# Performance work log

Measured on AMD Instinct MI355X. Metric: run time of the kernel, lower is better.

Reference implementation:

```python
import jax, jax.numpy as jnp
import numpy as np

D_IN = 2048
D_OUT = 2048
NUM_HEADS = 16
NUM_GROUPS = 4
HEAD_DIM = D_OUT // NUM_HEADS          # 128
HEADS_PER_GROUP = NUM_HEADS // NUM_GROUPS  # 4


def setup_inputs() -> dict:
    key = jax.random.key(0)
    ks = jax.random.split(key, 6)
    b, s = 2, 2048
    x = jax.random.normal(ks[0], (b, s, D_IN), dtype=jnp.float32)
    # Store weights as [in, out] so y = x @ W (equivalent to torch Linear x @ W.T)
    sc_q = 1.0 / np.sqrt(D_IN)
    Wq = jax.random.uniform(ks[1], (D_IN, D_OUT), jnp.float32, -sc_q, sc_q)
    Wk = jax.random.uniform(ks[2], (D_IN, NUM_GROUPS * HEAD_DIM), jnp.float32, -sc_q, sc_q)
    Wv = jax.random.uniform(ks[3], (D_IN, NUM_GROUPS * HEAD_DIM), jnp.float32, -sc_q, sc_q)
    sc_o = 1.0 / np.sqrt(D_OUT)
    Wo = jax.random.uniform(ks[4], (D_OUT, D_OUT), jnp.float32, -sc_o, sc_o)
    bo = jax.random.uniform(ks[5], (D_OUT,), jnp.float32, -sc_o, sc_o)
    return {"x": x, "Wq": Wq, "Wk": Wk, "Wv": Wv, "Wo": Wo, "bo": bo}


def reference(x, Wq, Wk, Wv, Wo, bo):
    b, s, _ = x.shape
    g, hpg, hd = NUM_GROUPS, HEADS_PER_GROUP, HEAD_DIM
    # Projections; keep grouped layout instead of repeat_interleave (same math)
    q = (x @ Wq).reshape(b, s, g, hpg, hd)   # query heads ordered group-major,
                                             # matching repeat_interleave of K/V
    k = (x @ Wk).reshape(b, s, g, hd)
    v = (x @ Wv).reshape(b, s, g, hd)
    # scores: [b, g, hpg, q_len, k_len]
    scores = jnp.einsum('bqghd,bkgd->bghqk', q, k)
    causal = jnp.triu(jnp.ones((s, s), dtype=bool), k=1)  # True above diagonal
    scores = jnp.where(causal, -jnp.inf, scores)
    scale = 1.0 / jnp.sqrt(jnp.asarray(hd, dtype=scores.dtype))
    attn = jax.nn.softmax(scores * scale, axis=-1)
    ctx = jnp.einsum('bghqk,bkgd->bqghd', attn, v).reshape(b, s, D_OUT)
    return ctx @ Wo + bo
```

## Files before the change

kernel.cpp:

```cpp
#include <hip/hip_runtime.h>

typedef short v8s __attribute__((ext_vector_type(8)));
typedef float v4f __attribute__((ext_vector_type(4)));

__device__ __forceinline__ short f2bf(float f) {
  union { float f; unsigned u; } v; v.f = f;
  unsigned r = v.u + 0x7FFFu + ((v.u >> 16) & 1u);
  return (short)(r >> 16);
}

__device__ __forceinline__ void gll16(const short* g, short* l) {
  __builtin_amdgcn_global_load_lds(
      (const __attribute__((address_space(1))) void*)g,
      (__attribute__((address_space(3))) void*)l, 16, 0, 0);
}

__global__ void cast_and_transpose(const float* __restrict__ x, short* __restrict__ xb,
                                   const float* __restrict__ Wq, const float* __restrict__ Wk,
                                   const float* __restrict__ Wv, const float* __restrict__ Wo,
                                   short* __restrict__ Wqkvt, short* __restrict__ Wot) {
  const int tid = threadIdx.x;
  int bid = blockIdx.x;
  if (bid < 8192) {
    int i = bid * 256 + tid;
    float4 v = ((const float4*)x)[i];
    short4 o;
    o.x = f2bf(v.x); o.y = f2bf(v.y); o.z = f2bf(v.z); o.w = f2bf(v.w);
    ((short4*)xb)[i] = o;
    return;
  }
  __shared__ float tile[32][33];
  bid -= 8192;
  const int tx = tid & 31, ty = tid >> 5;
  int bx = bid % 160;
  const int byy = bid / 160;
  const float* src; short* dst; int C, cb;
  if (bx < 64)      { src = Wq; dst = Wqkvt;                        C = 2048; cb = bx; }
  else if (bx < 80) { src = Wk; dst = Wqkvt + (size_t)2048 * 2048;  C = 512;  cb = bx - 64; }
  else if (bx < 96) { src = Wv; dst = Wqkvt + (size_t)2560 * 2048;  C = 512;  cb = bx - 80; }
  else              { src = Wo; dst = Wot;                          C = 2048; cb = bx - 96; }
  const int c0 = cb * 32, r0 = byy * 32;
#pragma unroll
  for (int i = 0; i < 4; ++i)
    tile[ty + 8 * i][tx] = src[(size_t)(r0 + ty + 8 * i) * C + c0 + tx];
  __syncthreads();
#pragma unroll
  for (int i = 0; i < 4; ++i)
    dst[(size_t)(c0 + ty + 8 * i) * 2048 + r0 + tx] = f2bf(tile[tx][ty + 8 * i]);
}

__global__ void transpose_v_perm(const short* __restrict__ qkv, short* __restrict__ out) {
  __shared__ short tile[32][33];
  const int tx = threadIdx.x, ty = threadIdx.y;
  const int c0 = blockIdx.x * 32, r0 = blockIdx.y * 32;
  const int z = blockIdx.z;
#pragma unroll
  for (int i = 0; i < 4; ++i)
    tile[ty + 8 * i][tx] = qkv[(size_t)(z * 2048 + r0 + ty + 8 * i) * 3072 + 2560 + c0 + tx];
  __syncthreads();
#pragma unroll
  for (int i = 0; i < 4; ++i) {
    int k = r0 + tx;
    int pk = (k & ~31) | ((((k >> 2) & 3) * 2 + ((k >> 4) & 1)) * 4) | (k & 3);
    out[(size_t)z * 512 * 2048 + (size_t)(c0 + ty + 8 * i) * 2048 + pk] = tile[tx][ty + 8 * i];
  }
}

template <int BF16_OUT>
__global__ __launch_bounds__(256, 3) void gemm_bt2p(const short* __restrict__ A,
                                                    const short* __restrict__ Bt,
                                                    void* __restrict__ Cout,
                                                    const float* __restrict__ bias,
                                                    int N, int K, int nbx, int cpx) {
  __shared__ __align__(16) short sm[2 * 8192];
  const int tid = threadIdx.x;
  const int w = tid >> 6, lane = tid & 63, quad = lane >> 4, l16 = lane & 15;
  const int wm = (w >> 1) * 64, wn = (w & 1) * 64;
  const int bid = blockIdx.x;
  const int swz = (bid & 7) * cpx + (bid >> 3);
  const int n0 = (swz % nbx) * 128, m0 = (swz / nbx) * 128;
  const int NT = K >> 5;

  const int srow = lane >> 2;
  const int sc = ((lane & 3) ^ ((lane >> 2) & 3) ^ ((lane >> 4) & 3)) * 8;
  const short* Ag = A + (size_t)(m0 + w * 16 + srow) * K + sc;
  const short* Bg = Bt + (size_t)(n0 + w * 16 + srow) * K + sc;
  short* Ad = sm + w * 512 + lane * 8;
  short* Bd = sm + 4096 + w * 512 + lane * 8;
  const size_t rjump = (size_t)64 * K;

  auto stage = [&](int t, int bf_) {
    const int k = t << 5;
    short* ad = Ad + bf_ * 8192;
    short* bd = Bd + bf_ * 8192;
    gll16(Ag + k, ad);
    gll16(Ag + k + rjump, ad + 2048);
    gll16(Bg + k, bd);
    gll16(Bg + k + rjump, bd + 2048);
  };

  const int rsc = (quad ^ (l16 & 3) ^ ((l16 >> 2) & 3)) * 8;
  const short* aBase = sm + (wm + l16) * 32 + rsc;
  const short* bBase = sm + 4096 + (wn + l16) * 32 + rsc;

  v4f acc[4][4] = {};

  stage(0, 0);
  __syncthreads();

  for (int t = 0; t < NT; ++t) {
    if (t + 1 < NT) stage(t + 1, (t + 1) & 1);
    const int bo_ = (t & 1) * 8192;
    v8s af[4], bf[4];
#pragma unroll
    for (int i = 0; i < 4; ++i) af[i] = *(const v8s*)(aBase + bo_ + i * 512);
#pragma unroll
    for (int i = 0; i < 4; ++i) bf[i] = *(const v8s*)(bBase + bo_ + i * 512);
    __builtin_amdgcn_s_setprio(1);
#pragma unroll
    for (int mi = 0; mi < 4; ++mi)
#pragma unroll
      for (int ni = 0; ni < 4; ++ni)
        acc[mi][ni] = __builtin_amdgcn_mfma_f32_16x16x32_bf16(af[mi], bf[ni], acc[mi][ni], 0, 0, 0);
    __builtin_amdgcn_s_setprio(0);
    if (t + 1 < NT) __syncthreads();
  }

#pragma unroll
  for (int mi = 0; mi < 4; ++mi) {
#pragma unroll
    for (int ni = 0; ni < 4; ++ni) {
      const int col = n0 + wn + ni * 16 + l16;
#pragma unroll
      for (int r = 0; r < 4; ++r) {
        const int row = m0 + wm + mi * 16 + quad * 4 + r;
        if (BF16_OUT) {
          ((short*)Cout)[(size_t)row * N + col] = f2bf(acc[mi][ni][r]);
        } else {
          ((float*)Cout)[(size_t)row * N + col] = acc[mi][ni][r] + bias[col];
        }
      }
    }
  }
}

__global__ __launch_bounds__(256, 2) void flash_attn4(const short* __restrict__ QKV,
                                                      const short* __restrict__ Vtb,
                                                      short* __restrict__ ctx) {
  __shared__ __align__(16) short smem[32768];
  const int tid = threadIdx.x;
  const int w = tid >> 6, lane = tid & 63, quad = lane >> 4, l16 = lane & 15;
  const int wq = w >> 1, wk = w & 1;
  const int bh = blockIdx.y;
  const int b = bh >> 4, h = bh & 15, g = h >> 2;
  const float scale = 0.08838834764831845f;
  v8s ones;
#pragma unroll
  for (int i = 0; i < 8; ++i) ones[i] = (short)0x3F80;

  const int krl = lane >> 4, kcl = lane & 15;
  const int vrl = lane >> 3, vcl = lane & 7;
  const short* Kg0 = QKV + (size_t)(b * 2048 + w * 16 + krl) * 3072 + 2048 + g * 128;
  const short* Vg0 = Vtb + (size_t)(b * 512 + g * 128 + w * 32 + vrl) * 2048 + (vcl ^ (vrl & 7)) * 8;
  short* kd = smem + (w * 16) * 128 + lane * 8;
  short* vd = smem + 8192 + (w * 32) * 64 + lane * 8;

  auto stage = [&](int key0, int bs) {
    const short* kg = Kg0 + (size_t)key0 * 3072;
    const short* vg = Vg0 + key0;
#pragma unroll
    for (int ii = 0; ii < 4; ++ii) {
      const int rl = (ii * 4 + krl) & 15;
      gll16(kg + (size_t)(ii * 4) * 3072 + (kcl ^ rl) * 8, kd + bs * 16384 + ii * 512);
      gll16(vg + (size_t)(ii * 8) * 2048, vd + bs * 16384 + ii * 512);
    }
  };

  float* red = (float*)smem;

#pragma unroll 1
  for (int half = 0; half < 2; ++half) {
    const int qt = half ? (31 - blockIdx.x) : blockIdx.x;
    const int q0 = qt * 64;
    const int qb = q0 + wq * 32;

    v8s aq[2][4];
#pragma unroll
    for (int qs = 0; qs < 2; ++qs) {
      const short* Qp = QKV + (size_t)(b * 2048 + qb + qs * 16 + l16) * 3072 + h * 128 + quad * 8;
#pragma unroll
      for (int kk = 0; kk < 4; ++kk) aq[qs][kk] = *(const v8s*)(Qp + kk * 32);
    }
    v4f o[2][8] = {};
    v4f ol[2] = {};

    __syncthreads();
    stage(0, 0);
    const int nk = qt + 1;
#pragma unroll 1
    for (int kt = 0; kt < nk; ++kt) {
      const int key0 = kt << 6;
      __syncthreads();
      if (kt + 1 < nk) stage((kt + 1) << 6, (kt + 1) & 1);
      const short* Ks = smem + (kt & 1) * 16384;
      const short* Vs = Ks + 8192;
      const int kb = key0 + wk * 32;
      if (kb > qb + 31) continue;
      v4f sf[2][2] = {};
      __builtin_amdgcn_s_setprio(1);
#pragma unroll
      for (int kfl = 0; kfl < 2; ++kfl)
#pragma unroll
        for (int kk = 0; kk < 4; ++kk) {
          v8s kfr = *(const v8s*)&Ks[((wk * 2 + kfl) * 16 + l16) * 128 + (((kk * 4 + quad) ^ l16) * 8)];
#pragma unroll
          for (int qs = 0; qs < 2; ++qs)
            sf[qs][kfl] = __builtin_amdgcn_mfma_f32_16x16x32_bf16(kfr, aq[qs][kk], sf[qs][kfl], 0, 0, 0);
        }
      __builtin_amdgcn_s_setprio(0);
      const bool diag = (kb + 31 > qb);
      v8s pa[2];
#pragma unroll
      for (int qs = 0; qs < 2; ++qs) {
        const int qg = qb + qs * 16 + l16;
        v8s t;
#pragma unroll
        for (int kfl = 0; kfl < 2; ++kfl)
#pragma unroll
          for (int r = 0; r < 4; ++r) {
            float s = sf[qs][kfl][r] * scale;
            if (diag && (kb + kfl * 16 + quad * 4 + r > qg)) s = -1e30f;
            t[kfl * 4 + r] = f2bf(__expf(s));
          }
        pa[qs] = t;
      }
      __builtin_amdgcn_s_setprio(1);
#pragma unroll
      for (int nf = 0; nf < 8; ++nf) {
        v8s vf = *(const v8s*)&Vs[(nf * 16 + l16) * 64 + (((wk * 4 + quad) ^ (l16 & 7)) * 8)];
#pragma unroll
        for (int qs = 0; qs < 2; ++qs)
          o[qs][nf] = __builtin_amdgcn_mfma_f32_16x16x32_bf16(pa[qs], vf, o[qs][nf], 0, 0, 0);
      }
#pragma unroll
      for (int qs = 0; qs < 2; ++qs)
        ol[qs] = __builtin_amdgcn_mfma_f32_16x16x32_bf16(pa[qs], ones, ol[qs], 0, 0, 0);
      __builtin_amdgcn_s_setprio(0);
    }
    __syncthreads();

    if (wk == 1) {
#pragma unroll
      for (int qs = 0; qs < 2; ++qs)
        *(v4f*)&red[(wq * 2 + qs) * 256 + l16 * 16 + quad * 4] = ol[qs];
    }
    __syncthreads();
    if (wk == 0) {
#pragma unroll
      for (int qs = 0; qs < 2; ++qs)
        ol[qs] += *(const v4f*)&red[(wq * 2 + qs) * 256 + l16 * 16 + quad * 4];
    }
    __syncthreads();
    if (wk == 1) {
#pragma unroll
      for (int qs = 0; qs < 2; ++qs)
#pragma unroll
        for (int nf = 0; nf < 8; ++nf)
          *(v4f*)&red[(((wq * 2 + qs) * 8 + nf) * 256) + l16 * 16 + quad * 4] = o[qs][nf];
    }
    __syncthreads();
    if (wk == 0) {
#pragma unroll
      for (int qs = 0; qs < 2; ++qs) {
        float inv[4];
#pragma unroll
        for (int r = 0; r < 4; ++r) inv[r] = 1.0f / ol[qs][r];
#pragma unroll
        for (int nf = 0; nf < 8; ++nf) {
          v4f osum = o[qs][nf] + *(const v4f*)&red[(((wq * 2 + qs) * 8 + nf) * 256) + l16 * 16 + quad * 4];
#pragma unroll
          for (int r = 0; r < 4; ++r) {
            const int row = qb + qs * 16 + quad * 4 + r;
            ctx[(size_t)(b * 2048 + row) * 2048 + h * 128 + nf * 16 + l16] = f2bf(osum[r] * inv[r]);
          }
        }
      }
    }
  }
}

extern "C" void kernel_launch(void* const* d_in, const int* in_sizes, int n_in,
                              void* d_out, int out_size, void* d_ws, size_t ws_size,
                              hipStream_t stream) {
  const float* x = (const float*)d_in[0];
  const float* Wq = (const float*)d_in[1];
  const float* Wk = (const float*)d_in[2];
  const float* Wv = (const float*)d_in[3];
  const float* Wo = (const float*)d_in[4];
  const float* bo = (const float*)d_in[5];
  float* out = (float*)d_out;
  char* ws = (char*)d_ws;

  short* xb    = (short*)(ws);
  short* ctx   = (short*)(ws);
  short* Wqkvt = (short*)(ws + 16777216);
  short* Wot   = (short*)(ws + 29360128);
  short* QKV   = (short*)(ws + 37748736);
  short* Vtb   = (short*)(ws + 62914560);

  cast_and_transpose<<<18432, 256, 0, stream>>>(x, xb, Wq, Wk, Wv, Wo, Wqkvt, Wot);

  gemm_bt2p<1><<<768, 256, 0, stream>>>(xb, Wqkvt, (void*)QKV, nullptr, 3072, 2048, 24, 96);

  transpose_v_perm<<<dim3(16, 64, 2), dim3(32, 8), 0, stream>>>(QKV, Vtb);

  flash_attn4<<<dim3(16, 32), 256, 0, stream>>>(QKV, Vtb, ctx);

  gemm_bt2p<0><<<512, 256, 0, stream>>>(ctx, Wot, (void*)out, bo, 2048, 2048, 16, 64);
}
```

Before: 288.9 us.

## Split attention work across eight waves with 16 query rows each

The flash-attention kernel grows from 4 to 8 waves per block. Each wave now owns 16 query rows instead of 32, which halves the accumulator and Q-fragment register footprint, and the K/V staging is redistributed so each wave loads fewer rows. The aim is more resident waves per CU to hide latency. The cost is that each K/V fragment read from LDS now feeds one MFMA instead of two, roughly doubling LDS read traffic per unit of math, and there are more waves contending at each barrier. The softmax scale is also folded with log2(e) so the kernel uses exp2f.

```diff
diff --git a/kernel.cpp b/kernel.cpp
--- a/kernel.cpp
+++ b/kernel.cpp
@@ -144,7 +144,7 @@
   }
 }
 
-__global__ __launch_bounds__(256, 2) void flash_attn4(const short* __restrict__ QKV,
+__global__ __launch_bounds__(512, 4) void flash_attn6(const short* __restrict__ QKV,
                                                       const short* __restrict__ Vtb,
                                                       short* __restrict__ ctx) {
   __shared__ __align__(16) short smem[32768];
@@ -153,24 +153,24 @@
   const int wq = w >> 1, wk = w & 1;
   const int bh = blockIdx.y;
   const int b = bh >> 4, h = bh & 15, g = h >> 2;
-  const float scale = 0.08838834764831845f;
+  const float k2e = 0.08838834764831845f * 1.4426950408889634f;
   v8s ones;
 #pragma unroll
   for (int i = 0; i < 8; ++i) ones[i] = (short)0x3F80;
 
   const int krl = lane >> 4, kcl = lane & 15;
   const int vrl = lane >> 3, vcl = lane & 7;
-  const short* Kg0 = QKV + (size_t)(b * 2048 + w * 16 + krl) * 3072 + 2048 + g * 128;
-  const short* Vg0 = Vtb + (size_t)(b * 512 + g * 128 + w * 32 + vrl) * 2048 + (vcl ^ (vrl & 7)) * 8;
-  short* kd = smem + (w * 16) * 128 + lane * 8;
-  short* vd = smem + 8192 + (w * 32) * 64 + lane * 8;
+  const short* Kg0 = QKV + (size_t)(b * 2048 + w * 8 + krl) * 3072 + 2048 + g * 128;
+  const short* Vg0 = Vtb + (size_t)(b * 512 + g * 128 + w * 16 + vrl) * 2048 + (vcl ^ (vrl & 7)) * 8;
+  short* kd = smem + (w * 8) * 128 + lane * 8;
+  short* vd = smem + 8192 + (w * 16) * 64 + lane * 8;
 
   auto stage = [&](int key0, int bs) {
     const short* kg = Kg0 + (size_t)key0 * 3072;
     const short* vg = Vg0 + key0;
 #pragma unroll
-    for (int ii = 0; ii < 4; ++ii) {
-      const int rl = (ii * 4 + krl) & 15;
+    for (int ii = 0; ii < 2; ++ii) {
+      const int rl = (w & 1) * 8 + ii * 4 + krl;
       gll16(kg + (size_t)(ii * 4) * 3072 + (kcl ^ rl) * 8, kd + bs * 16384 + ii * 512);
       gll16(vg + (size_t)(ii * 8) * 2048, vd + bs * 16384 + ii * 512);
     }
@@ -182,17 +182,16 @@
   for (int half = 0; half < 2; ++half) {
     const int qt = half ? (31 - blockIdx.x) : blockIdx.x;
     const int q0 = qt * 64;
-    const int qb = q0 + wq * 32;
-
-    v8s aq[2][4];
-#pragma unroll
-    for (int qs = 0; qs < 2; ++qs) {
-      const short* Qp = QKV + (size_t)(b * 2048 + qb + qs * 16 + l16) * 3072 + h * 128 + quad * 8;
-#pragma unroll
-      for (int kk = 0; kk < 4; ++kk) aq[qs][kk] = *(const v8s*)(Qp + kk * 32);
-    }
-    v4f o[2][8] = {};
-    v4f ol[2] = {};
+    const int qb = q0 + wq * 16;
+
+    v8s aq[4];
+    {
+      const short* Qp = QKV + (size_t)(b * 2048 + qb + l16) * 3072 + h * 128 + quad * 8;
+#pragma unroll
+      for (int kk = 0; kk < 4; ++kk) aq[kk] = *(const v8s*)(Qp + kk * 32);
+    }
+    v4f o[8] = {};
+    v4f ol = {};
 
     __syncthreads();
     stage(0, 0);
@@ -205,84 +204,62 @@
       const short* Ks = smem + (kt & 1) * 16384;
       const short* Vs = Ks + 8192;
       const int kb = key0 + wk * 32;
-      if (kb > qb + 31) continue;
-      v4f sf[2][2] = {};
+      if (kb > qb + 15) continue;
+      v4f sf[2] = {};
       __builtin_amdgcn_s_setprio(1);
 #pragma unroll
       for (int kfl = 0; kfl < 2; ++kfl)
 #pragma unroll
         for (int kk = 0; kk < 4; ++kk) {
           v8s kfr = *(const v8s*)&Ks[((wk * 2 + kfl) * 16 + l16) * 128 + (((kk * 4 + quad) ^ l16) * 8)];
-#pragma unroll
-          for (int qs = 0; qs < 2; ++qs)
-            sf[qs][kfl] = __builtin_amdgcn_mfma_f32_16x16x32_bf16(kfr, aq[qs][kk], sf[qs][kfl], 0, 0, 0);
+          sf[kfl] = __builtin_amdgcn_mfma_f32_16x16x32_bf16(kfr, aq[kk], sf[kfl], 0, 0, 0);
         }
       __builtin_amdgcn_s_setprio(0);
       const bool diag = (kb + 31 > qb);
-      v8s pa[2];
-#pragma unroll
-      for (int qs = 0; qs < 2; ++qs) {
-        const int qg = qb + qs * 16 + l16;
-        v8s t;
-#pragma unroll
-        for (int kfl = 0; kfl < 2; ++kfl)
-#pragma unroll
-          for (int r = 0; r < 4; ++r) {
-            float s = sf[qs][kfl][r] * scale;
-            if (diag && (kb + kfl * 16 + quad * 4 + r > qg)) s = -1e30f;
-            t[kfl * 4 + r] = f2bf(__expf(s));
-          }
-        pa[qs] = t;
-      }
+      const int qg = qb + l16;
+      v8s pa;
+#pragma unroll
+      for (int kfl = 0; kfl < 2; ++kfl)
+#pragma unroll
+        for (int r = 0; r < 4; ++r) {
+          float s = sf[kfl][r];
+          if (diag && (kb + kfl * 16 + quad * 4 + r > qg)) s = -1e30f;
+          pa[kfl * 4 + r] = f2bf(exp2f(s * k2e));
+        }
       __builtin_amdgcn_s_setprio(1);
 #pragma unroll
       for (int nf = 0; nf < 8; ++nf) {
         v8s vf = *(const v8s*)&Vs[(nf * 16 + l16) * 64 + (((wk * 4 + quad) ^ (l16 & 7)) * 8)];
-#pragma unroll
-        for (int qs = 0; qs < 2; ++qs)
-          o[qs][nf] = __builtin_amdgcn_mfma_f32_16x16x32_bf16(pa[qs], vf, o[qs][nf], 0, 0, 0);
+        o[nf] = __builtin_amdgcn_mfma_f32_16x16x32_bf16(pa, vf, o[nf], 0, 0, 0);
       }
-#pragma unroll
-      for (int qs = 0; qs < 2; ++qs)
-        ol[qs] = __builtin_amdgcn_mfma_f32_16x16x32_bf16(pa[qs], ones, ol[qs], 0, 0, 0);
+      ol = __builtin_amdgcn_mfma_f32_16x16x32_bf16(pa, ones, ol, 0, 0, 0);
       __builtin_amdgcn_s_setprio(0);
     }
     __syncthreads();
 
+    if (wk == 1)
+      *(v4f*)&red[wq * 256 + l16 * 16 + quad * 4] = ol;
+    __syncthreads();
+    if (wk == 0)
+      ol += *(const v4f*)&red[wq * 256 + l16 * 16 + quad * 4];
+    __syncthreads();
     if (wk == 1) {
 #pragma unroll
-      for (int qs = 0; qs < 2; ++qs)
-        *(v4f*)&red[(wq * 2 + qs) * 256 + l16 * 16 + quad * 4] = ol[qs];
+      for (int nf = 0; nf < 8; ++nf)
+        *(v4f*)&red[(wq * 8 + nf) * 256 + l16 * 16 + quad * 4] = o[nf];
     }
     __syncthreads();
     if (wk == 0) {
-#pragma unroll
-      for (int qs = 0; qs < 2; ++qs)
-        ol[qs] += *(const v4f*)&red[(wq * 2 + qs) * 256 + l16 * 16 + quad * 4];
-    }
-    __syncthreads();
-    if (wk == 1) {
-#pragma unroll
-      for (int qs = 0; qs < 2; ++qs)
-#pragma unroll
-        for (int nf = 0; nf < 8; ++nf)
-          *(v4f*)&red[(((wq * 2 + qs) * 8 + nf) * 256) + l16 * 16 + quad * 4] = o[qs][nf];
-    }
-    __syncthreads();
-    if (wk == 0) {
-#pragma unroll
-      for (int qs = 0; qs < 2; ++qs) {
-        float inv[4];
-#pragma unroll
-        for (int r = 0; r < 4; ++r) inv[r] = 1.0f / ol[qs][r];
-#pragma unroll
-        for (int nf = 0; nf < 8; ++nf) {
-          v4f osum = o[qs][nf] + *(const v4f*)&red[(((wq * 2 + qs) * 8 + nf) * 256) + l16 * 16 + quad * 4];
-#pragma unroll
-          for (int r = 0; r < 4; ++r) {
-            const int row = qb + qs * 16 + quad * 4 + r;
-            ctx[(size_t)(b * 2048 + row) * 2048 + h * 128 + nf * 16 + l16] = f2bf(osum[r] * inv[r]);
-          }
+      float inv[4];
+#pragma unroll
+      for (int r = 0; r < 4; ++r) inv[r] = 1.0f / ol[r];
+#pragma unroll
+      for (int nf = 0; nf < 8; ++nf) {
+        v4f osum = o[nf] + *(const v4f*)&red[(wq * 8 + nf) * 256 + l16 * 16 + quad * 4];
+#pragma unroll
+        for (int r = 0; r < 4; ++r) {
+          const int row = qb + quad * 4 + r;
+          ctx[(size_t)(b * 2048 + row) * 2048 + h * 128 + nf * 16 + l16] = f2bf(osum[r] * inv[r]);
         }
       }
     }
@@ -314,7 +291,7 @@
 
   transpose_v_perm<<<dim3(16, 64, 2), dim3(32, 8), 0, stream>>>(QKV, Vtb);
 
-  flash_attn4<<<dim3(16, 32), 256, 0, stream>>>(QKV, Vtb, ctx);
+  flash_attn6<<<dim3(16, 32), 512, 0, stream>>>(QKV, Vtb, ctx);
 
   gemm_bt2p<0><<<512, 256, 0, stream>>>(ctx, Wot, (void*)out, bo, 2048, 2048, 16, 64);
 }
```

Measured after the change: 279.4 us. 3.3% less time.

## Use 8-wave attention blocks with 128-query tiles and prescale Wq for exp2

Applied to the files above, without the earlier changes.

The flash attention kernel goes from 4 to 8 waves per block, each block covering 128 query rows instead of 64, so each staged K/V tile is shared by twice as many query rows and global K/V traffic per query drops. The softmax scale and log2(e) are folded into Wq during the weight cast, so the inner loop can call exp2f without a multiply. The bf16 conversion of P now uses the packed hardware instruction v_cvt_pk_bf16_f32 instead of the software rounding routine. Risks include fewer blocks to fill the GPU, more causally masked waste on diagonal tiles, and the unseen epilogue or reduction code possibly still assuming 4 waves.

```diff
diff --git a/kernel.cpp b/kernel.cpp
--- a/kernel.cpp
+++ b/kernel.cpp
@@ -34,8 +34,9 @@
   const int tx = tid & 31, ty = tid >> 5;
   int bx = bid % 160;
   const int byy = bid / 160;
-  const float* src; short* dst; int C, cb;
-  if (bx < 64)      { src = Wq; dst = Wqkvt;                        C = 2048; cb = bx; }
+  const float* src; short* dst; int C, cb; float fac = 1.0f;
+  if (bx < 64)      { src = Wq; dst = Wqkvt;                        C = 2048; cb = bx;
+                      fac = 0.08838834764831845f * 1.4426950408889634f; }
   else if (bx < 80) { src = Wk; dst = Wqkvt + (size_t)2048 * 2048;  C = 512;  cb = bx - 64; }
   else if (bx < 96) { src = Wv; dst = Wqkvt + (size_t)2560 * 2048;  C = 512;  cb = bx - 80; }
   else              { src = Wo; dst = Wot;                          C = 2048; cb = bx - 96; }
@@ -46,7 +47,7 @@
   __syncthreads();
 #pragma unroll
   for (int i = 0; i < 4; ++i)
-    dst[(size_t)(c0 + ty + 8 * i) * 2048 + r0 + tx] = f2bf(tile[tx][ty + 8 * i]);
+    dst[(size_t)(c0 + ty + 8 * i) * 2048 + r0 + tx] = f2bf(tile[tx][ty + 8 * i] * fac);
 }
 
 __global__ void transpose_v_perm(const short* __restrict__ qkv, short* __restrict__ out) {
@@ -144,7 +145,7 @@
   }
 }
 
-__global__ __launch_bounds__(256, 2) void flash_attn4(const short* __restrict__ QKV,
+__global__ __launch_bounds__(512, 2) void flash_attn8(const short* __restrict__ QKV,
                                                       const short* __restrict__ Vtb,
                                                       short* __restrict__ ctx) {
   __shared__ __align__(16) short smem[32768];
@@ -153,24 +154,23 @@
   const int wq = w >> 1, wk = w & 1;
   const int bh = blockIdx.y;
   const int b = bh >> 4, h = bh & 15, g = h >> 2;
-  const float scale = 0.08838834764831845f;
   v8s ones;
 #pragma unroll
   for (int i = 0; i < 8; ++i) ones[i] = (short)0x3F80;
 
   const int krl = lane >> 4, kcl = lane & 15;
   const int vrl = lane >> 3, vcl = lane & 7;
-  const short* Kg0 = QKV + (size_t)(b * 2048 + w * 16 + krl) * 3072 + 2048 + g * 128;
-  const short* Vg0 = Vtb + (size_t)(b * 512 + g * 128 + w * 32 + vrl) * 2048 + (vcl ^ (vrl & 7)) * 8;
-  short* kd = smem + (w * 16) * 128 + lane * 8;
-  short* vd = smem + 8192 + (w * 32) * 64 + lane * 8;
+  const short* Kg0 = QKV + (size_t)(b * 2048 + w * 8 + krl) * 3072 + 2048 + g * 128;
+  const short* Vg0 = Vtb + (size_t)(b * 512 + g * 128 + w * 16 + vrl) * 2048 + (vcl ^ (vrl & 7)) * 8;
+  short* kd = smem + (w * 8) * 128 + lane * 8;
+  short* vd = smem + 8192 + (w * 16) * 64 + lane * 8;
 
   auto stage = [&](int key0, int bs) {
     const short* kg = Kg0 + (size_t)key0 * 3072;
     const short* vg = Vg0 + key0;
 #pragma unroll
-    for (int ii = 0; ii < 4; ++ii) {
-      const int rl = (ii * 4 + krl) & 15;
+    for (int ii = 0; ii < 2; ++ii) {
+      const int rl = (w & 1) * 8 + ii * 4 + krl;
       gll16(kg + (size_t)(ii * 4) * 3072 + (kcl ^ rl) * 8, kd + bs * 16384 + ii * 512);
       gll16(vg + (size_t)(ii * 8) * 2048, vd + bs * 16384 + ii * 512);
     }
@@ -180,8 +180,8 @@
 
 #pragma unroll 1
   for (int half = 0; half < 2; ++half) {
-    const int qt = half ? (31 - blockIdx.x) : blockIdx.x;
-    const int q0 = qt * 64;
+    const int qt = half ? (15 - blockIdx.x) : blockIdx.x;
+    const int q0 = qt * 128;
     const int qb = q0 + wq * 32;
 
     v8s aq[2][4];
@@ -196,7 +196,7 @@
 
     __syncthreads();
     stage(0, 0);
-    const int nk = qt + 1;
+    const int nk = 2 * qt + 2;
 #pragma unroll 1
     for (int kt = 0; kt < nk; ++kt) {
       const int key0 = kt << 6;
@@ -223,16 +223,20 @@
 #pragma unroll
       for (int qs = 0; qs < 2; ++qs) {
         const int qg = qb + qs * 16 + l16;
-        v8s t;
-#pragma unroll
-        for (int kfl = 0; kfl < 2; ++kfl)
+        union { v8s v; unsigned u[4]; } pu;
+#pragma unroll
+        for (int kfl = 0; kfl < 2; ++kfl) {
+          float e[4];
 #pragma unroll
           for (int r = 0; r < 4; ++r) {
-            float s = sf[qs][kfl][r] * scale;
+            float s = sf[qs][kfl][r];
             if (diag && (kb + kfl * 16 + quad * 4 + r > qg)) s = -1e30f;
-            t[kfl * 4 + r] = f2bf(__expf(s));
+            e[r] = exp2f(s);
           }
-        pa[qs] = t;
+          asm("v_cvt_pk_bf16_f32 %0, %1, %2" : "=v"(pu.u[kfl * 2 + 0]) : "v"(e[0]), "v"(e[1]));
+          asm("v_cvt_pk_bf16_f32 %0, %1, %2" : "=v"(pu.u[kfl * 2 + 1]) : "v"(e[2]), "v"(e[3]));
+        }
+        pa[qs] = pu.v;
       }
       __builtin_amdgcn_s_setprio(1);
 #pragma unroll
@@ -314,7 +318,7 @@
 
   transpose_v_perm<<<dim3(16, 64, 2), dim3(32, 8), 0, stream>>>(QKV, Vtb);
 
-  flash_attn4<<<dim3(16, 32), 256, 0, stream>>>(QKV, Vtb, ctx);
+  flash_attn8<<<dim3(8, 32), 512, 0, stream>>>(QKV, Vtb, ctx);
 
   gemm_bt2p<0><<<512, 256, 0, stream>>>(ctx, Wot, (void*)out, bo, 2048, 2048, 16, 64);
 }
```

New measurement: 279.5 us. 1.03x faster.
